# Optimization experiments

Hardware: AMD Instinct MI355X
Metric: run time of the kernel (lower is better)

The kernel has to match this reference:

```python
import jax, jax.numpy as jnp
import numpy as np

B, NS, S, H = 512, 2, 128, 768
DS, NL = 384, 40
TEMP, ALPHA, GAMMA = 0.05, 0.15, 7.5
EPS = 1e-8


def setup_inputs() -> dict:
    key = jax.random.key(0)
    ks = jax.random.split(key, 8)
    return {
        "bert_emb": jax.random.normal(ks[0], (B, NS, S, H), dtype=jnp.float32),
        "rel_desc_emb": jax.random.normal(ks[1], (B, DS), dtype=jnp.float32),
        "dense_w": 0.02 * jax.random.normal(ks[2], (H, H), dtype=jnp.float32),
        "dense_b": jnp.zeros((H,), dtype=jnp.float32),
        "cls_w": 0.02 * jax.random.normal(ks[3], (3 * H, NL), dtype=jnp.float32),
        "cls_b": jnp.zeros((NL,), dtype=jnp.float32),
        "fc_w": 0.02 * jax.random.normal(ks[4], (3 * H, DS), dtype=jnp.float32),
        "fc_b": jnp.zeros((DS,), dtype=jnp.float32),
        "entity_idx": jax.random.randint(ks[5], (B, NS, 2), 0, S, dtype=jnp.int64 if jax.config.jax_enable_x64 else jnp.int32),
        "classify_labels": jax.random.randint(ks[6], (B,), 0, NL, dtype=jnp.int64 if jax.config.jax_enable_x64 else jnp.int32),
    }


def _mean_ce(logits, labels):
    lp = jax.nn.log_softmax(logits, axis=-1)
    return -jnp.mean(jnp.take_along_axis(lp, labels[:, None], axis=1))


def _l2n(x):
    return x / jnp.maximum(jnp.linalg.norm(x, axis=-1, keepdims=True), EPS)


def reference(bert_emb, rel_desc_emb, dense_w, dense_b, cls_w, cls_b, fc_w, fc_b,
              entity_idx, classify_labels):
    b = bert_emb.shape[0]
    bidx = jnp.arange(b)
    # ----- relation representation from sentence 0 (cls | head | tail) -----
    s0 = bert_emb[:, 0]                                   # [B,S,H]
    cls_tok = s0[:, 0]                                    # [B,H]
    head = s0[bidx, entity_idx[:, 0, 0]]                  # [B,H]
    tail = s0[bidx, entity_idx[:, 0, 1]]                  # [B,H]
    relation_hidden = jnp.tanh(jnp.concatenate([cls_tok, head, tail], axis=-1))  # [B,3H]
    logits = relation_hidden @ cls_w + cls_b              # [B,NL]
    ce_loss = _mean_ce(logits, classify_labels)
    # ----- margin loss vs relation-description embeddings (cosine) -----
    rel_emb = relation_hidden @ fc_w + fc_b               # [B,DS]
    C = _l2n(rel_emb) @ _l2n(rel_desc_emb).T              # [B,B] cosine sims
    pos = jnp.diagonal(C)
    diff_label = classify_labels[:, None] != classify_labels[None, :]
    neg = jnp.max(jnp.where(diff_label, C, -jnp.inf), axis=1)
    neg = jnp.maximum(neg, 0.0)                           # max_val initialized at 0
    margin_loss = jnp.sum(jax.nn.relu(neg - pos + GAMMA)) * (1.0 - ALPHA)
    ce_loss = ce_loss + margin_loss
    # ----- contrastive loss on (head|tail) entity pairs from both sents -----
    # dense is token-wise; apply only to the 4 gathered tokens per example
    h1a = bert_emb[bidx, 0, entity_idx[:, 0, 0]]
    h1b = bert_emb[bidx, 0, entity_idx[:, 0, 1]]
    h2a = bert_emb[bidx, 1, entity_idx[:, 1, 0]]
    h2b = bert_emb[bidx, 1, entity_idx[:, 1, 1]]
    toks = jnp.stack([h1a, h1b, h2a, h2b], axis=1)        # [B,4,H]
    toks = jnp.tanh(toks @ dense_w + dense_b)             # [B,4,H]
    z1 = toks[:, 0:2].reshape(b, -1)                      # [B,2H]
    z2 = toks[:, 2:4].reshape(b, -1)                      # [B,2H]
    cos_sim = (_l2n(z1) @ _l2n(z2).T) / TEMP              # [B,B]
    cl_loss = _mean_ce(cos_sim, bidx)
    return ce_loss + ALPHA * cl_loss
```

## Files before the change

### kernel.cpp

```cpp
#include <hip/hip_runtime.h>
#include <hip/hip_bf16.h>
#include <math.h>

#define B_   512
#define NS_  2
#define S_   128
#define H_   768
#define DS_  384
#define NL_  40
#define H3_  (3*H_)
#define TEMP_ 0.05f
#define ALPHA_ 0.15f
#define GAMMA_ 7.5f
#define EPS_ 1e-8f

typedef __attribute__((ext_vector_type(8))) short bf8_t;
typedef __attribute__((ext_vector_type(4))) float f4_t;

#define LDSPAD 40


__device__ __forceinline__ float block_reduce_sum(float v, float* sh) {
    int t = threadIdx.x;
    sh[t] = v; __syncthreads();
    for (int s = blockDim.x / 2; s > 0; s >>= 1) {
        if (t < s) sh[t] += sh[t + s];
        __syncthreads();
    }
    float r = sh[0]; __syncthreads();
    return r;
}

__device__ __forceinline__ float block_reduce_max(float v, float* sh) {
    int t = threadIdx.x;
    sh[t] = v; __syncthreads();
    for (int s = blockDim.x / 2; s > 0; s >>= 1) {
        if (t < s) sh[t] = fmaxf(sh[t], sh[t + s]);
        __syncthreads();
    }
    float r = sh[0]; __syncthreads();
    return r;
}

__device__ __forceinline__ void transpose_tile(
    const float* __restrict__ in, __hip_bfloat16* __restrict__ out,
    int K, int N, int kt, int nt, int tid, float* tileLds )
{
    int k0 = kt * 32, n0 = nt * 32;
    int tx = tid & 31, ty = tid >> 5;
#pragma unroll
    for (int i = 0; i < 4; ++i) {
        int k = k0 + ty + i * 8, n = n0 + tx;
        if (k < K && n < N) tileLds[(ty + i*8) * 33 + tx] = in[(size_t)k * N + n];
    }
    __syncthreads();
#pragma unroll
    for (int i = 0; i < 4; ++i) {
        int n = n0 + ty + i * 8, k = k0 + tx;
        if (n < N && k < K) out[(size_t)n * K + k] = __float2bfloat16(tileLds[tx * 33 + ty + i*8]);
    }
}

__global__ __launch_bounds__(256) void prep_kernel(
    const float* __restrict__ bert, const int* __restrict__ eidx,
    const float* __restrict__ dense_w, const float* __restrict__ fc_w,
    const float* __restrict__ cls_w,
    __hip_bfloat16* __restrict__ rh_bf, __hip_bfloat16* __restrict__ toks_bf,
    __hip_bfloat16* __restrict__ dwt, __hip_bfloat16* __restrict__ fwt,
    __hip_bfloat16* __restrict__ cwt, float* __restrict__ acc)
{
    __shared__ float tileLds[32 * 33];
    int blk = blockIdx.x;
    int t = threadIdx.x;
    if (blk < 512) {
        int b = blk;
        if (b == 0 && t < 4) acc[t] = 0.0f;
        int e00 = eidx[b*4 + 0];
        int e01 = eidx[b*4 + 1];
        int e10 = eidx[b*4 + 2];
        int e11 = eidx[b*4 + 3];
        const float* s0 = bert + (size_t)b * NS_ * S_ * H_;
        const float* s1 = s0 + (size_t)S_ * H_;
        const float* cls  = s0;
        const float* head = s0 + (size_t)e00 * H_;
        const float* tail = s0 + (size_t)e01 * H_;
        const float* h2a  = s1 + (size_t)e10 * H_;
        const float* h2b  = s1 + (size_t)e11 * H_;
        __hip_bfloat16* rhb = rh_bf + (size_t)b * H3_;
        __hip_bfloat16* tk  = toks_bf + (size_t)b * 4 * H_;
        for (int h = t; h < H_; h += 256) {
            float c  = cls[h];
            float hd = head[h];
            float tl = tail[h];
            rhb[h]        = __float2bfloat16(tanhf(c));
            rhb[H_ + h]   = __float2bfloat16(tanhf(hd));
            rhb[2*H_ + h] = __float2bfloat16(tanhf(tl));
            tk[h]         = __float2bfloat16(hd);
            tk[H_ + h]    = __float2bfloat16(tl);
            tk[2*H_ + h]  = __float2bfloat16(h2a[h]);
            tk[3*H_ + h]  = __float2bfloat16(h2b[h]);
        }
    } else if (blk < 1088) {
        int q = blk - 512;
        transpose_tile(dense_w, dwt, H_, H_, q / 24, q % 24, t, tileLds);
    } else if (blk < 1952) {
        int q = blk - 1088;
        transpose_tile(fc_w, fwt, H3_, DS_, q / 12, q % 12, t, tileLds);
    } else {
        int q = blk - 1952;
        transpose_tile(cls_w, cwt, H3_, NL_, q / 2, q % 2, t, tileLds);
    }
}

__global__ __launch_bounds__(256) void mfma_abt128(
    const __hip_bfloat16* __restrict__ A, const __hip_bfloat16* __restrict__ Bp,
    const float* __restrict__ bias, float* __restrict__ C,
    int K, int lda, int ldb, int ldc, int fuse_tanh)
{
    __shared__ __hip_bfloat16 As[128 * LDSPAD];
    __shared__ __hip_bfloat16 Bs[128 * LDSPAD];
    int tid  = threadIdx.x;
    int lane = tid & 63;
    int wave = tid >> 6;
    int wm = (wave >> 1) * 64;
    int wn = (wave & 1) * 64;
    int lr = lane & 15;
    int quad = lane >> 4;
    int rowBase = blockIdx.y * 128;
    int colBase = blockIdx.x * 128;

    f4_t acc[4][4];
#pragma unroll
    for (int i = 0; i < 4; ++i)
#pragma unroll
        for (int j = 0; j < 4; ++j) acc[i][j] = (f4_t){0.f, 0.f, 0.f, 0.f};

    int sr = tid >> 2, sc = tid & 3;
    for (int k0 = 0; k0 < K; k0 += 32) {
#pragma unroll
        for (int half = 0; half < 2; ++half) {
            int r = sr + half * 64;
            *(bf8_t*)&As[r * LDSPAD + sc * 8] =
                *(const bf8_t*)(A + (size_t)(rowBase + r) * lda + k0 + sc * 8);
            *(bf8_t*)&Bs[r * LDSPAD + sc * 8] =
                *(const bf8_t*)(Bp + (size_t)(colBase + r) * ldb + k0 + sc * 8);
        }
        __syncthreads();
        bf8_t af[4], bfr[4];
#pragma unroll
        for (int f = 0; f < 4; ++f) {
            af[f]  = *(const bf8_t*)&As[(wm + f*16 + lr) * LDSPAD + quad * 8];
            bfr[f] = *(const bf8_t*)&Bs[(wn + f*16 + lr) * LDSPAD + quad * 8];
        }
#pragma unroll
        for (int i = 0; i < 4; ++i)
#pragma unroll
            for (int j = 0; j < 4; ++j)
                acc[i][j] = __builtin_amdgcn_mfma_f32_16x16x32_bf16(af[i], bfr[j], acc[i][j], 0, 0, 0);
        __syncthreads();
    }
#pragma unroll
    for (int j = 0; j < 4; ++j) {
        int col = colBase + wn + j*16 + lr;
        float bv = bias ? bias[col] : 0.0f;
#pragma unroll
        for (int i = 0; i < 4; ++i) {
            int row0 = rowBase + wm + i*16 + quad*4;
#pragma unroll
            for (int r = 0; r < 4; ++r) {
                float v = acc[i][j][r] + bv;
                if (fuse_tanh) v = tanhf(v);
                C[(size_t)(row0 + r) * ldc + col] = v;
            }
        }
    }
}

__global__ __launch_bounds__(256) void mfma_abt64(
    const __hip_bfloat16* __restrict__ A, const __hip_bfloat16* __restrict__ Bp,
    const float* __restrict__ bias, float* __restrict__ C,
    int K, int lda, int ldb, int ldc, float scale)
{
    __shared__ __hip_bfloat16 As[64 * LDSPAD];
    __shared__ __hip_bfloat16 Bs[64 * LDSPAD];
    int tid  = threadIdx.x;
    int lane = tid & 63;
    int wave = tid >> 6;
    int lr = lane & 15;
    int quad = lane >> 4;
    int rowBase = blockIdx.y * 64;
    int colBase = blockIdx.x * 64;

    f4_t acc[4];
#pragma unroll
    for (int i = 0; i < 4; ++i) acc[i] = (f4_t){0.f, 0.f, 0.f, 0.f};

    int sr = tid >> 2, sc = tid & 3;
    for (int k0 = 0; k0 < K; k0 += 32) {
        *(bf8_t*)&As[sr * LDSPAD + sc * 8] =
            *(const bf8_t*)(A + (size_t)(rowBase + sr) * lda + k0 + sc * 8);
        *(bf8_t*)&Bs[sr * LDSPAD + sc * 8] =
            *(const bf8_t*)(Bp + (size_t)(colBase + sr) * ldb + k0 + sc * 8);
        __syncthreads();
        bf8_t bfr = *(const bf8_t*)&Bs[(wave*16 + lr) * LDSPAD + quad * 8];
#pragma unroll
        for (int f = 0; f < 4; ++f) {
            bf8_t af = *(const bf8_t*)&As[(f*16 + lr) * LDSPAD + quad * 8];
            acc[f] = __builtin_amdgcn_mfma_f32_16x16x32_bf16(af, bfr, acc[f], 0, 0, 0);
        }
        __syncthreads();
    }
    int col = colBase + wave*16 + lr;
    float bv = bias ? bias[col] : 0.0f;
#pragma unroll
    for (int f = 0; f < 4; ++f) {
        int row0 = rowBase + f*16 + quad*4;
#pragma unroll
        for (int r = 0; r < 4; ++r)
            C[(size_t)(row0 + r) * ldc + col] = acc[f][r] * scale + bv;
    }
}

__global__ __launch_bounds__(256) void cls_ce_fused(
    const __hip_bfloat16* __restrict__ rh, const __hip_bfloat16* __restrict__ cwt,
    const float* __restrict__ cls_b, const int* __restrict__ labels,
    float* __restrict__ acc)
{
    __shared__ __hip_bfloat16 As[64 * LDSPAD];
    __shared__ __hip_bfloat16 Bs[48 * LDSPAD];
    __shared__ float lg[64 * 48];
    __shared__ float shred[64];
    int tid  = threadIdx.x;
    int lane = tid & 63;
    int wave = tid >> 6;
    int lr = lane & 15;
    int quad = lane >> 4;
    int rowBase = blockIdx.x * 64;

    f4_t a3[3];
#pragma unroll
    for (int j = 0; j < 3; ++j) a3[j] = (f4_t){0.f, 0.f, 0.f, 0.f};

    int sr = tid >> 2, sc = tid & 3;
    for (int k0 = 0; k0 < H3_; k0 += 32) {
        *(bf8_t*)&As[sr * LDSPAD + sc * 8] =
            *(const bf8_t*)(rh + (size_t)(rowBase + sr) * H3_ + k0 + sc * 8);
        if (tid < 192) {
            bf8_t v = (sr < NL_) ? *(const bf8_t*)(cwt + (size_t)sr * H3_ + k0 + sc * 8)
                                 : (bf8_t){0,0,0,0,0,0,0,0};
            *(bf8_t*)&Bs[sr * LDSPAD + sc * 8] = v;
        }
        __syncthreads();
        bf8_t af = *(const bf8_t*)&As[(wave*16 + lr) * LDSPAD + quad * 8];
#pragma unroll
        for (int j = 0; j < 3; ++j) {
            bf8_t bfr = *(const bf8_t*)&Bs[(j*16 + lr) * LDSPAD + quad * 8];
            a3[j] = __builtin_amdgcn_mfma_f32_16x16x32_bf16(af, bfr, a3[j], 0, 0, 0);
        }
        __syncthreads();
    }
#pragma unroll
    for (int j = 0; j < 3; ++j) {
        int col = j*16 + lr;
        float bv = (col < NL_) ? cls_b[col] : 0.0f;
#pragma unroll
        for (int r = 0; r < 4; ++r) {
            int rowl = wave*16 + quad*4 + r;
            lg[rowl * 48 + col] = (col < NL_) ? (a3[j][r] + bv) : -INFINITY;
        }
    }
    __syncthreads();
    if (tid < 64) {
        const float* Lr = &lg[tid * 48];
        float m = -INFINITY;
        for (int c = 0; c < NL_; ++c) m = fmaxf(m, Lr[c]);
        float s = 0.0f;
        for (int c = 0; c < NL_; ++c) s += expf(Lr[c] - m);
        int lbl = labels[rowBase + tid];
        shred[tid] = logf(s) + m - Lr[lbl];
    }
    __syncthreads();
    if (tid < 32) shred[tid] += shred[tid + 32];
    __syncthreads();
    if (tid < 16) shred[tid] += shred[tid + 16];
    __syncthreads();
    if (tid < 8) shred[tid] += shred[tid + 8];
    __syncthreads();
    if (tid == 0) {
        float s = 0.0f;
        for (int i = 0; i < 8; ++i) s += shred[i];
        atomicAdd(acc + 0, s * (1.0f / (float)B_));
    }
}

__global__ __launch_bounds__(256) void norms_kernel(
    const float* __restrict__ desc, const float* __restrict__ rel_emb,
    const float* __restrict__ toks_out,
    __hip_bfloat16* __restrict__ desc_nb, __hip_bfloat16* __restrict__ rel_nb,
    __hip_bfloat16* __restrict__ z_bf)
{
    __shared__ float sh[256];
    int blk = blockIdx.x, t = threadIdx.x;
    const float* x; __hip_bfloat16* o; int D;
    if (blk < 512)       { x = desc + (size_t)blk * DS_;            o = desc_nb + (size_t)blk * DS_;            D = DS_; }
    else if (blk < 1024) { x = rel_emb + (size_t)(blk-512) * DS_;   o = rel_nb + (size_t)(blk-512) * DS_;       D = DS_; }
    else                 { x = toks_out + (size_t)(blk-1024)*2*H_;  o = z_bf + (size_t)(blk-1024)*2*H_;         D = 2*H_; }
    float ss = 0.0f;
    for (int d = t; d < D; d += 256) { float v = x[d]; ss += v * v; }
    ss = block_reduce_sum(ss, sh);
    float inv = 1.0f / fmaxf(sqrtf(ss), EPS_);
    for (int d = t; d < D; d += 256) o[d] = __float2bfloat16(x[d] * inv);
}

__global__ __launch_bounds__(256) void tail_kernel(
    const float* __restrict__ C1, const float* __restrict__ C2,
    const int* __restrict__ labels, float* __restrict__ acc)
{
    __shared__ float sh[256];
    int blk = blockIdx.x, t = threadIdx.x;
    if (blk < 512) {
        int i = blk;
        int li = labels[i];
        const float* row = C1 + (size_t)i * B_;
        float m = -INFINITY;
        for (int j = t; j < B_; j += 256)
            if (labels[j] != li) m = fmaxf(m, row[j]);
        float negmax = block_reduce_max(m, sh);
        if (t == 0) {
            float neg = fmaxf(negmax, 0.0f);
            float term = neg - row[i] + GAMMA_;
            if (term > 0.0f) atomicAdd(acc + 1, term);
        }
    } else {
        int i = blk - 512;
        const float* row = C2 + (size_t)i * B_;
        float m = -INFINITY;
        for (int j = t; j < B_; j += 256) m = fmaxf(m, row[j]);
        m = block_reduce_max(m, sh);
        float s = 0.0f;
        for (int j = t; j < B_; j += 256) s += expf(row[j] - m);
        s = block_reduce_sum(s, sh);
        if (t == 0) atomicAdd(acc + 2, (logf(s) + m - row[i]) * (1.0f / (float)B_));
    }
}

__global__ void finalize(const float* __restrict__ acc, float* __restrict__ out) {
    if (threadIdx.x == 0 && blockIdx.x == 0)
        out[0] = acc[0] + (1.0f - ALPHA_) * acc[1] + ALPHA_ * acc[2];
}


extern "C" void kernel_launch(void* const* d_in, const int* in_sizes, int n_in,
                              void* d_out, int out_size, void* d_ws, size_t ws_size,
                              hipStream_t stream) {
    const float* bert     = (const float*)d_in[0];
    const float* desc     = (const float*)d_in[1];
    const float* dense_w  = (const float*)d_in[2];
    const float* dense_b  = (const float*)d_in[3];
    const float* cls_w    = (const float*)d_in[4];
    const float* cls_b    = (const float*)d_in[5];
    const float* fc_w     = (const float*)d_in[6];
    const float* fc_b     = (const float*)d_in[7];
    const int*   eidx     = (const int*)d_in[8];
    const int*   labels   = (const int*)d_in[9];
    float* out = (float*)d_out;

    float* fp = (float*)d_ws;
    __hip_bfloat16* rh_bf   = (__hip_bfloat16*)fp; fp += (size_t)B_*H3_/2;
    __hip_bfloat16* toks_bf = (__hip_bfloat16*)fp; fp += (size_t)B_*4*H_/2;
    __hip_bfloat16* dwt_bf  = (__hip_bfloat16*)fp; fp += (size_t)H_*H_/2;
    __hip_bfloat16* fwt_bf  = (__hip_bfloat16*)fp; fp += (size_t)DS_*H3_/2;
    __hip_bfloat16* cwt_bf  = (__hip_bfloat16*)fp; fp += (size_t)NL_*H3_/2;
    __hip_bfloat16* desc_nb = (__hip_bfloat16*)fp; fp += (size_t)B_*DS_/2;
    __hip_bfloat16* rel_nb  = (__hip_bfloat16*)fp; fp += (size_t)B_*DS_/2;
    __hip_bfloat16* z_bf    = (__hip_bfloat16*)fp; fp += (size_t)B_*4*H_/2;
    float* toks_out = fp; fp += (size_t)B_*4*H_;
    float* rel_emb  = fp; fp += (size_t)B_*DS_;
    float* C1       = fp; fp += (size_t)B_*B_;
    float* C2       = fp; fp += (size_t)B_*B_;
    float* acc      = fp;

    prep_kernel<<<2096, 256, 0, stream>>>(bert, eidx, dense_w, fc_w, cls_w,
                                          rh_bf, toks_bf, dwt_bf, fwt_bf, cwt_bf, acc);

    mfma_abt128<<<dim3(H_/128, (B_*4)/128), 256, 0, stream>>>(
        toks_bf, dwt_bf, dense_b, toks_out, H_, H_, H_, H_, 1);

    mfma_abt64<<<dim3(DS_/64, B_/64), 256, 0, stream>>>(
        rh_bf, fwt_bf, fc_b, rel_emb, H3_, H3_, H3_, DS_, 1.0f);

    cls_ce_fused<<<B_/64, 256, 0, stream>>>(rh_bf, cwt_bf, cls_b, labels, acc);

    norms_kernel<<<2048, 256, 0, stream>>>(desc, rel_emb, toks_out, desc_nb, rel_nb, z_bf);

    mfma_abt64<<<dim3(B_/64, B_/64), 256, 0, stream>>>(
        rel_nb, desc_nb, (const float*)nullptr, C1, DS_, DS_, DS_, B_, 1.0f);

    mfma_abt64<<<dim3(B_/64, B_/64), 256, 0, stream>>>(
        z_bf, z_bf + 2*H_, (const float*)nullptr, C2, 2*H_, 4*H_, 4*H_, B_, 1.0f/TEMP_);

    tail_kernel<<<1024, 256, 0, stream>>>(C1, C2, labels, acc);

    finalize<<<1, 64, 0, stream>>>(acc, out);
}
```

Before: 600.5 us.

## Merge independent GEMM launches into fused multi-role kernels and drop finalize launch

Cuts the launch count from nine to five. The dense, fc and classifier GEMMs now share one kernel, dispatched by block index, and the C1 and C2 similarity GEMMs share another. Description normalization moves into the prep kernel, and the finalize kernel is replaced by a last-block-done atomic counter inside the tail kernel. The classifier CE is reworked to use 16-row blocks that split K across waves, read operands straight from global memory with no LDS staging, and reduce partial sums in LDS, with cls_w zero-padded to 48 rows. This removes launch gaps and serialization between small kernels, at the cost of unbalanced block roles and a global atomic completion pattern.

New measurement: 569.9 us. 5.1% less time.

```diff
diff --git a/kernel.cpp b/kernel.cpp
--- a/kernel.cpp
+++ b/kernel.cpp
@@ -64,17 +64,21 @@
 __global__ __launch_bounds__(256) void prep_kernel(
     const float* __restrict__ bert, const int* __restrict__ eidx,
     const float* __restrict__ dense_w, const float* __restrict__ fc_w,
-    const float* __restrict__ cls_w,
+    const float* __restrict__ cls_w, const float* __restrict__ desc,
     __hip_bfloat16* __restrict__ rh_bf, __hip_bfloat16* __restrict__ toks_bf,
     __hip_bfloat16* __restrict__ dwt, __hip_bfloat16* __restrict__ fwt,
-    __hip_bfloat16* __restrict__ cwt, float* __restrict__ acc)
+    __hip_bfloat16* __restrict__ cwt, __hip_bfloat16* __restrict__ desc_nb,
+    float* __restrict__ acc, int* __restrict__ done)
 {
     __shared__ float tileLds[32 * 33];
     int blk = blockIdx.x;
     int t = threadIdx.x;
     if (blk < 512) {
         int b = blk;
-        if (b == 0 && t < 4) acc[t] = 0.0f;
+        if (b == 0) {
+            if (t < 4) acc[t] = 0.0f;
+            if (t == 4) *done = 0;
+        }
         int e00 = eidx[b*4 + 0];
         int e01 = eidx[b*4 + 1];
         int e10 = eidx[b*4 + 2];
@@ -106,19 +110,33 @@
     } else if (blk < 1952) {
         int q = blk - 1088;
         transpose_tile(fc_w, fwt, H3_, DS_, q / 12, q % 12, t, tileLds);
+    } else if (blk < 2096) {
+        int q = blk - 1952;
+        int kt = q / 2, nt = q % 2;
+        transpose_tile(cls_w, cwt, H3_, NL_, kt, nt, t, tileLds);
+        if (nt == 1) {
+            int tx = t & 31, ty = t >> 5;
+            cwt[(size_t)(40 + ty) * H3_ + kt * 32 + tx] = __float2bfloat16(0.0f);
+        }
     } else {
-        int q = blk - 1952;
-        transpose_tile(cls_w, cwt, H3_, NL_, q / 2, q % 2, t, tileLds);
-    }
-}
-
-__global__ __launch_bounds__(256) void mfma_abt128(
+        int i = blk - 2096;
+        const float* x = desc + (size_t)i * DS_;
+        float ss = 0.0f;
+        for (int d = t; d < DS_; d += 256) { float v = x[d]; ss += v * v; }
+        ss = block_reduce_sum(ss, tileLds);
+        float inv = 1.0f / fmaxf(sqrtf(ss), EPS_);
+        __hip_bfloat16* o = desc_nb + (size_t)i * DS_;
+        for (int d = t; d < DS_; d += 256) o[d] = __float2bfloat16(x[d] * inv);
+    }
+}
+
+
+__device__ __forceinline__ void gemm128_body(
     const __hip_bfloat16* __restrict__ A, const __hip_bfloat16* __restrict__ Bp,
     const float* __restrict__ bias, float* __restrict__ C,
-    int K, int lda, int ldb, int ldc, int fuse_tanh)
-{
-    __shared__ __hip_bfloat16 As[128 * LDSPAD];
-    __shared__ __hip_bfloat16 Bs[128 * LDSPAD];
+    int K, int lda, int ldb, int ldc, int fuse_tanh, int bx, int by,
+    __hip_bfloat16* As, __hip_bfloat16* Bs)
+{
     int tid  = threadIdx.x;
     int lane = tid & 63;
     int wave = tid >> 6;
@@ -126,8 +144,8 @@
     int wn = (wave & 1) * 64;
     int lr = lane & 15;
     int quad = lane >> 4;
-    int rowBase = blockIdx.y * 128;
-    int colBase = blockIdx.x * 128;
+    int rowBase = by * 128;
+    int colBase = bx * 128;
 
     f4_t acc[4][4];
 #pragma unroll
@@ -176,20 +194,19 @@
     }
 }
 
-__global__ __launch_bounds__(256) void mfma_abt64(
+__device__ __forceinline__ void gemm64_body(
     const __hip_bfloat16* __restrict__ A, const __hip_bfloat16* __restrict__ Bp,
     const float* __restrict__ bias, float* __restrict__ C,
-    int K, int lda, int ldb, int ldc, float scale)
-{
-    __shared__ __hip_bfloat16 As[64 * LDSPAD];
-    __shared__ __hip_bfloat16 Bs[64 * LDSPAD];
+    int K, int lda, int ldb, int ldc, float scale, int bx, int by,
+    __hip_bfloat16* As, __hip_bfloat16* Bs)
+{
     int tid  = threadIdx.x;
     int lane = tid & 63;
     int wave = tid >> 6;
     int lr = lane & 15;
     int quad = lane >> 4;
-    int rowBase = blockIdx.y * 64;
-    int colBase = blockIdx.x * 64;
+    int rowBase = by * 64;
+    int colBase = bx * 64;
 
     f4_t acc[4];
 #pragma unroll
@@ -221,90 +238,96 @@
     }
 }
 
-__global__ __launch_bounds__(256) void cls_ce_fused(
+__device__ __forceinline__ void cls_ce_body(
     const __hip_bfloat16* __restrict__ rh, const __hip_bfloat16* __restrict__ cwt,
     const float* __restrict__ cls_b, const int* __restrict__ labels,
-    float* __restrict__ acc)
-{
-    __shared__ __hip_bfloat16 As[64 * LDSPAD];
-    __shared__ __hip_bfloat16 Bs[48 * LDSPAD];
-    __shared__ float lg[64 * 48];
-    __shared__ float shred[64];
+    float* __restrict__ acc, int rowBase, float* lgp )
+{
     int tid  = threadIdx.x;
     int lane = tid & 63;
     int wave = tid >> 6;
     int lr = lane & 15;
     int quad = lane >> 4;
-    int rowBase = blockIdx.x * 64;
 
     f4_t a3[3];
 #pragma unroll
     for (int j = 0; j < 3; ++j) a3[j] = (f4_t){0.f, 0.f, 0.f, 0.f};
 
-    int sr = tid >> 2, sc = tid & 3;
-    for (int k0 = 0; k0 < H3_; k0 += 32) {
-        *(bf8_t*)&As[sr * LDSPAD + sc * 8] =
-            *(const bf8_t*)(rh + (size_t)(rowBase + sr) * H3_ + k0 + sc * 8);
-        if (tid < 192) {
-            bf8_t v = (sr < NL_) ? *(const bf8_t*)(cwt + (size_t)sr * H3_ + k0 + sc * 8)
-                                 : (bf8_t){0,0,0,0,0,0,0,0};
-            *(bf8_t*)&Bs[sr * LDSPAD + sc * 8] = v;
-        }
-        __syncthreads();
-        bf8_t af = *(const bf8_t*)&As[(wave*16 + lr) * LDSPAD + quad * 8];
+    int kw0 = wave * (H3_ / 4);
+    const __hip_bfloat16* aRow = rh + (size_t)(rowBase + lr) * H3_ + quad * 8;
+#pragma unroll 2
+    for (int s = 0; s < 18; ++s) {
+        int k = kw0 + s * 32;
+        bf8_t af = *(const bf8_t*)(aRow + k);
 #pragma unroll
         for (int j = 0; j < 3; ++j) {
-            bf8_t bfr = *(const bf8_t*)&Bs[(j*16 + lr) * LDSPAD + quad * 8];
+            bf8_t bfr = *(const bf8_t*)(cwt + (size_t)(j*16 + lr) * H3_ + k + quad * 8);
             a3[j] = __builtin_amdgcn_mfma_f32_16x16x32_bf16(af, bfr, a3[j], 0, 0, 0);
         }
-        __syncthreads();
     }
 #pragma unroll
     for (int j = 0; j < 3; ++j) {
         int col = j*16 + lr;
-        float bv = (col < NL_) ? cls_b[col] : 0.0f;
-#pragma unroll
-        for (int r = 0; r < 4; ++r) {
-            int rowl = wave*16 + quad*4 + r;
-            lg[rowl * 48 + col] = (col < NL_) ? (a3[j][r] + bv) : -INFINITY;
-        }
+#pragma unroll
+        for (int r = 0; r < 4; ++r)
+            lgp[wave * 768 + (quad*4 + r) * 48 + col] = a3[j][r];
+    }
+    __syncthreads();
+    for (int idx = tid; idx < 768; idx += 256) {
+        int col = idx % 48;
+        float s = lgp[idx] + lgp[768 + idx] + lgp[1536 + idx] + lgp[2304 + idx];
+        s = (col < NL_) ? (s + cls_b[col]) : -INFINITY;
+        lgp[idx] = s;
     }
     __syncthreads();
     if (tid < 64) {
-        const float* Lr = &lg[tid * 48];
-        float m = -INFINITY;
-        for (int c = 0; c < NL_; ++c) m = fmaxf(m, Lr[c]);
-        float s = 0.0f;
-        for (int c = 0; c < NL_; ++c) s += expf(Lr[c] - m);
-        int lbl = labels[rowBase + tid];
-        shred[tid] = logf(s) + m - Lr[lbl];
-    }
-    __syncthreads();
-    if (tid < 32) shred[tid] += shred[tid + 32];
-    __syncthreads();
-    if (tid < 16) shred[tid] += shred[tid + 16];
-    __syncthreads();
-    if (tid < 8) shred[tid] += shred[tid + 8];
-    __syncthreads();
-    if (tid == 0) {
-        float s = 0.0f;
-        for (int i = 0; i < 8; ++i) s += shred[i];
-        atomicAdd(acc + 0, s * (1.0f / (float)B_));
-    }
-}
-
-__global__ __launch_bounds__(256) void norms_kernel(
-    const float* __restrict__ desc, const float* __restrict__ rel_emb,
-    const float* __restrict__ toks_out,
-    __hip_bfloat16* __restrict__ desc_nb, __hip_bfloat16* __restrict__ rel_nb,
-    __hip_bfloat16* __restrict__ z_bf)
+        float ce = 0.0f;
+        if (tid < 16) {
+            const float* Lr = &lgp[tid * 48];
+            float m = -INFINITY;
+            for (int c = 0; c < NL_; ++c) m = fmaxf(m, Lr[c]);
+            float s = 0.0f;
+            for (int c = 0; c < NL_; ++c) s += expf(Lr[c] - m);
+            ce = logf(s) + m - Lr[labels[rowBase + tid]];
+        }
+        for (int off = 8; off >= 1; off >>= 1) ce += __shfl_down(ce, off);
+        if (tid == 0) atomicAdd(acc + 0, ce * (1.0f / (float)B_));
+    }
+}
+
+__global__ __launch_bounds__(256) void gemms_kernel(
+    const __hip_bfloat16* __restrict__ toks_bf, const __hip_bfloat16* __restrict__ dwt,
+    const float* __restrict__ dense_b, float* __restrict__ toks_out,
+    const __hip_bfloat16* __restrict__ rh_bf, const __hip_bfloat16* __restrict__ fwt,
+    const float* __restrict__ fc_b, float* __restrict__ rel_emb,
+    const __hip_bfloat16* __restrict__ cwt, const float* __restrict__ cls_b,
+    const int* __restrict__ labels, float* __restrict__ acc)
+{
+    __shared__ __align__(16) char smem[2 * 128 * LDSPAD * 2];
+    int blk = blockIdx.x;
+    if (blk < 96) {
+        gemm128_body(toks_bf, dwt, dense_b, toks_out, H_, H_, H_, H_, 1,
+                     blk % 6, blk / 6,
+                     (__hip_bfloat16*)smem, (__hip_bfloat16*)(smem + 128 * LDSPAD * 2));
+    } else if (blk < 144) {
+        int q = blk - 96;
+        gemm64_body(rh_bf, fwt, fc_b, rel_emb, H3_, H3_, H3_, DS_, 1.0f,
+                    q % 6, q / 6,
+                    (__hip_bfloat16*)smem, (__hip_bfloat16*)(smem + 64 * LDSPAD * 2));
+    } else {
+        cls_ce_body(rh_bf, cwt, cls_b, labels, acc, (blk - 144) * 16, (float*)smem);
+    }
+}
+
+__global__ __launch_bounds__(256) void znorm_kernel(
+    const float* __restrict__ rel_emb, const float* __restrict__ toks_out,
+    __hip_bfloat16* __restrict__ rel_nb, __hip_bfloat16* __restrict__ z_bf)
 {
     __shared__ float sh[256];
     int blk = blockIdx.x, t = threadIdx.x;
     const float* x; __hip_bfloat16* o; int D;
-    if (blk < 512)       { x = desc + (size_t)blk * DS_;            o = desc_nb + (size_t)blk * DS_;            D = DS_; }
-    else if (blk < 1024) { x = rel_emb + (size_t)(blk-512) * DS_;   o = rel_nb + (size_t)(blk-512) * DS_;       D = DS_; }
-    else                 { x = toks_out + (size_t)(blk-1024)*2*H_;  o = z_bf + (size_t)(blk-1024)*2*H_;         D = 2*H_; }
+    if (blk < 512) { x = rel_emb + (size_t)blk * DS_;          o = rel_nb + (size_t)blk * DS_;        D = DS_; }
+    else           { x = toks_out + (size_t)(blk-512) * 2*H_;  o = z_bf + (size_t)(blk-512) * 2*H_;   D = 2*H_; }
     float ss = 0.0f;
     for (int d = t; d < D; d += 256) { float v = x[d]; ss += v * v; }
     ss = block_reduce_sum(ss, sh);
@@ -312,9 +335,28 @@
     for (int d = t; d < D; d += 256) o[d] = __float2bfloat16(x[d] * inv);
 }
 
+__global__ __launch_bounds__(256) void c1c2_kernel(
+    const __hip_bfloat16* __restrict__ rel_nb, const __hip_bfloat16* __restrict__ desc_nb,
+    const __hip_bfloat16* __restrict__ z_bf, float* __restrict__ C1, float* __restrict__ C2)
+{
+    __shared__ __align__(16) char smem[2 * 64 * LDSPAD * 2];
+    __hip_bfloat16* As = (__hip_bfloat16*)smem;
+    __hip_bfloat16* Bs = (__hip_bfloat16*)(smem + 64 * LDSPAD * 2);
+    int blk = blockIdx.x;
+    if (blk < 64) {
+        gemm64_body(rel_nb, desc_nb, (const float*)nullptr, C1, DS_, DS_, DS_, B_, 1.0f,
+                    blk % 8, blk / 8, As, Bs);
+    } else {
+        int q = blk - 64;
+        gemm64_body(z_bf, z_bf + 2*H_, (const float*)nullptr, C2, 2*H_, 4*H_, 4*H_, B_, 1.0f/TEMP_,
+                    q % 8, q / 8, As, Bs);
+    }
+}
+
 __global__ __launch_bounds__(256) void tail_kernel(
     const float* __restrict__ C1, const float* __restrict__ C2,
-    const int* __restrict__ labels, float* __restrict__ acc)
+    const int* __restrict__ labels, float* __restrict__ acc,
+    int* __restrict__ done, float* __restrict__ out)
 {
     __shared__ float sh[256];
     int blk = blockIdx.x, t = threadIdx.x;
@@ -342,11 +384,16 @@
         s = block_reduce_sum(s, sh);
         if (t == 0) atomicAdd(acc + 2, (logf(s) + m - row[i]) * (1.0f / (float)B_));
     }
-}
-
-__global__ void finalize(const float* __restrict__ acc, float* __restrict__ out) {
-    if (threadIdx.x == 0 && blockIdx.x == 0)
-        out[0] = acc[0] + (1.0f - ALPHA_) * acc[1] + ALPHA_ * acc[2];
+    __threadfence();
+    if (t == 0) {
+        int prev = atomicAdd(done, 1);
+        if (prev == 1023) {
+            float a0 = atomicAdd(acc + 0, 0.0f);
+            float a1 = atomicAdd(acc + 1, 0.0f);
+            float a2 = atomicAdd(acc + 2, 0.0f);
+            out[0] = a0 + (1.0f - ALPHA_) * a1 + ALPHA_ * a2;
+        }
+    }
 }
 
 
@@ -370,7 +417,7 @@
     __hip_bfloat16* toks_bf = (__hip_bfloat16*)fp; fp += (size_t)B_*4*H_/2;
     __hip_bfloat16* dwt_bf  = (__hip_bfloat16*)fp; fp += (size_t)H_*H_/2;
     __hip_bfloat16* fwt_bf  = (__hip_bfloat16*)fp; fp += (size_t)DS_*H3_/2;
-    __hip_bfloat16* cwt_bf  = (__hip_bfloat16*)fp; fp += (size_t)NL_*H3_/2;
+    __hip_bfloat16* cwt_bf  = (__hip_bfloat16*)fp; fp += (size_t)48*H3_/2;
     __hip_bfloat16* desc_nb = (__hip_bfloat16*)fp; fp += (size_t)B_*DS_/2;
     __hip_bfloat16* rel_nb  = (__hip_bfloat16*)fp; fp += (size_t)B_*DS_/2;
     __hip_bfloat16* z_bf    = (__hip_bfloat16*)fp; fp += (size_t)B_*4*H_/2;
@@ -378,28 +425,20 @@
     float* rel_emb  = fp; fp += (size_t)B_*DS_;
     float* C1       = fp; fp += (size_t)B_*B_;
     float* C2       = fp; fp += (size_t)B_*B_;
-    float* acc      = fp;
-
-    prep_kernel<<<2096, 256, 0, stream>>>(bert, eidx, dense_w, fc_w, cls_w,
-                                          rh_bf, toks_bf, dwt_bf, fwt_bf, cwt_bf, acc);
-
-    mfma_abt128<<<dim3(H_/128, (B_*4)/128), 256, 0, stream>>>(
-        toks_bf, dwt_bf, dense_b, toks_out, H_, H_, H_, H_, 1);
-
-    mfma_abt64<<<dim3(DS_/64, B_/64), 256, 0, stream>>>(
-        rh_bf, fwt_bf, fc_b, rel_emb, H3_, H3_, H3_, DS_, 1.0f);
-
-    cls_ce_fused<<<B_/64, 256, 0, stream>>>(rh_bf, cwt_bf, cls_b, labels, acc);
-
-    norms_kernel<<<2048, 256, 0, stream>>>(desc, rel_emb, toks_out, desc_nb, rel_nb, z_bf);
-
-    mfma_abt64<<<dim3(B_/64, B_/64), 256, 0, stream>>>(
-        rel_nb, desc_nb, (const float*)nullptr, C1, DS_, DS_, DS_, B_, 1.0f);
-
-    mfma_abt64<<<dim3(B_/64, B_/64), 256, 0, stream>>>(
-        z_bf, z_bf + 2*H_, (const float*)nullptr, C2, 2*H_, 4*H_, 4*H_, B_, 1.0f/TEMP_);
-
-    tail_kernel<<<1024, 256, 0, stream>>>(C1, C2, labels, acc);
-
-    finalize<<<1, 64, 0, stream>>>(acc, out);
-}
+    float* acc      = fp; fp += 4;
+    int*   done     = (int*)fp;
+
+    prep_kernel<<<2608, 256, 0, stream>>>(bert, eidx, dense_w, fc_w, cls_w, desc,
+                                          rh_bf, toks_bf, dwt_bf, fwt_bf, cwt_bf,
+                                          desc_nb, acc, done);
+
+    gemms_kernel<<<176, 256, 0, stream>>>(toks_bf, dwt_bf, dense_b, toks_out,
+                                          rh_bf, fwt_bf, fc_b, rel_emb,
+                                          cwt_bf, cls_b, labels, acc);
+
+    znorm_kernel<<<1536, 256, 0, stream>>>(rel_emb, toks_out, rel_nb, z_bf);
+
+    c1c2_kernel<<<128, 256, 0, stream>>>(rel_nb, desc_nb, z_bf, C1, C2);
+
+    tail_kernel<<<1024, 256, 0, stream>>>(C1, C2, labels, acc, done, out);
+}
```
